# Optimization experiments

Measured on AMD Instinct MI355X. Metric: run time of the kernel, lower is better.

The kernel has to match this reference:

```python
import jax, jax.numpy as jnp
import numpy as np

N = 100000
E = 640000
D_IN = 128
D_OUT = 128
EPS = 0.0


def setup_inputs() -> dict:
    key = jax.random.key(0)
    k1, k2, k3, k4, k5, k6 = jax.random.split(key, 6)
    x = jax.random.normal(k1, (N, D_IN), dtype=jnp.float32)
    edge_index = jax.random.randint(k2, (2, E), 0, N, dtype=jnp.int64)
    # MLP params (Linear(in,out) -> ReLU -> Linear(out,out)), PyTorch-style init scale
    s1 = 1.0 / np.sqrt(D_IN)
    s2 = 1.0 / np.sqrt(D_OUT)
    W1 = jax.random.uniform(k3, (D_IN, D_OUT), minval=-s1, maxval=s1, dtype=jnp.float32)
    b1 = jax.random.uniform(k4, (D_OUT,), minval=-s1, maxval=s1, dtype=jnp.float32)
    W2 = jax.random.uniform(k5, (D_OUT, D_OUT), minval=-s2, maxval=s2, dtype=jnp.float32)
    b2 = jax.random.uniform(k6, (D_OUT,), minval=-s2, maxval=s2, dtype=jnp.float32)
    return {"x": x, "edge_index": edge_index, "W1": W1, "b1": b1, "W2": W2, "b2": b2}


def reference(x, edge_index, W1, b1, W2, b2):
    row, col = edge_index[0], edge_index[1]
    # gather source features, scatter-add into destination nodes
    aggregated = jax.ops.segment_sum(x[row], col, num_segments=N)  # [N, D_IN]
    h = (1.0 + EPS) * x + aggregated
    h = jnp.maximum(h @ W1 + b1, 0.0)
    return h @ W2 + b2
```

## Files before the change

### kernel.cpp

```cpp
#include <hip/hip_runtime.h>

#define NN 100000
#define EE 640000
#define DD 128
#define NB 391

typedef short bf16x8 __attribute__((ext_vector_type(8)));
typedef float f32x4 __attribute__((ext_vector_type(4)));

__device__ __forceinline__ unsigned short f2bf(float f) {
    union { float f; unsigned int u; } a; a.f = f;
    unsigned int u = a.u + 0x7fffu + ((a.u >> 16) & 1u);
    return (unsigned short)(u >> 16);
}

__device__ __forceinline__ int wave_incl_scan(int v, int lane) {
#pragma unroll
    for (int d = 1; d < 64; d <<= 1) {
        int u = __shfl_up(v, d, 64);
        if (lane >= d) v += u;
    }
    return v;
}

__global__ __launch_bounds__(256) void k_hist(const int* __restrict__ ei,
                                              int* __restrict__ deg) {
    int e = blockIdx.x * 256 + threadIdx.x;
    if (e >= EE) return;
    atomicAdd(&deg[ei[EE + e]], 1);
}

__global__ __launch_bounds__(256) void k_scan1(const int* __restrict__ deg,
                                               int* __restrict__ bsum) {
    int i = blockIdx.x * 256 + threadIdx.x;
    int v = (i < NN) ? deg[i] : 0;
#pragma unroll
    for (int d = 32; d; d >>= 1) v += __shfl_down(v, d, 64);
    __shared__ int wsum[4];
    if ((threadIdx.x & 63) == 0) wsum[threadIdx.x >> 6] = v;
    __syncthreads();
    if (threadIdx.x == 0) bsum[blockIdx.x] = wsum[0] + wsum[1] + wsum[2] + wsum[3];
}

__global__ __launch_bounds__(512) void k_scan2(int* __restrict__ bsum,
                                               int* __restrict__ offs) {
    int t = threadIdx.x, lane = t & 63, w = t >> 6;
    int v = (t < NB) ? bsum[t] : 0;
    int s = wave_incl_scan(v, lane);
    __shared__ int wsum[8];
    if (lane == 63) wsum[w] = s;
    __syncthreads();
    int off = 0;
    for (int k = 0; k < w; ++k) off += wsum[k];
    if (t < NB) bsum[t] = off + s - v;
    if (t == 0) offs[NN] = EE;
}

__global__ __launch_bounds__(256) void k_scan3(const int* __restrict__ deg,
                                               const int* __restrict__ bsum,
                                               int* __restrict__ offs) {
    int t = threadIdx.x, lane = t & 63, w = t >> 6;
    int i = blockIdx.x * 256 + t;
    int v = (i < NN) ? deg[i] : 0;
    int s = wave_incl_scan(v, lane);
    __shared__ int wsum[4];
    if (lane == 63) wsum[w] = s;
    __syncthreads();
    int off = bsum[blockIdx.x];
    for (int k = 0; k < w; ++k) off += wsum[k];
    if (i < NN) offs[i] = off + s - v;
}

__global__ __launch_bounds__(256) void k_fill(const int* __restrict__ ei,
                                              int* __restrict__ deg,
                                              const int* __restrict__ offs,
                                              int* __restrict__ bucket) {
    int e = blockIdx.x * 256 + threadIdx.x;
    if (e >= EE) return;
    int r = ei[e];
    int c = ei[EE + e];
    int p = atomicSub(&deg[c], 1) - 1;
    bucket[offs[c] + p] = r;
}

__global__ __launch_bounds__(256) void k_gather(const float* __restrict__ x,
                                                const int* __restrict__ offs,
                                                const int* __restrict__ bucket,
                                                float* __restrict__ h0) {
    int gid = blockIdx.x * 256 + threadIdx.x;
    int n = gid >> 6;
    if (n >= NN) return;
    int lane = gid & 63;
    const float2* xr = reinterpret_cast<const float2*>(x);
    float2 acc = xr[(size_t)n * 64 + lane];
    int j = offs[n], jend = offs[n + 1];
    for (; j + 1 < jend; j += 2) {
        int a = bucket[j], b = bucket[j + 1];
        float2 va = xr[(size_t)a * 64 + lane];
        float2 vb = xr[(size_t)b * 64 + lane];
        acc.x += va.x + vb.x;
        acc.y += va.y + vb.y;
    }
    if (j < jend) {
        int a = bucket[j];
        float2 va = xr[(size_t)a * 64 + lane];
        acc.x += va.x;
        acc.y += va.y;
    }
    reinterpret_cast<float2*>(h0)[(size_t)n * 64 + lane] = acc;
}

__global__ __launch_bounds__(256) void k_prep(const float* __restrict__ W1,
                                              const float* __restrict__ W2,
                                              unsigned short* __restrict__ w1t,
                                              unsigned short* __restrict__ w2t) {
    int idx = blockIdx.x * 256 + threadIdx.x;
    if (idx >= 2 * DD * DD) return;
    const float* W = (idx < DD * DD) ? W1 : W2;
    unsigned short* O = (idx < DD * DD) ? w1t : w2t;
    int i = idx & (DD * DD - 1);
    int n = i >> 7, k = i & (DD - 1);
    O[i] = f2bf(W[k * DD + n]);
}

__global__ __launch_bounds__(256, 2) void k_mlp(const float* __restrict__ h0,
                                                const unsigned short* __restrict__ w1t,
                                                const unsigned short* __restrict__ w2t,
                                                const float* __restrict__ b1,
                                                const float* __restrict__ b2,
                                                float* __restrict__ out) {
    __shared__ unsigned short lds[DD * DD];
    const int t  = threadIdx.x;
    const int w  = t >> 6, l = t & 63;
    const int wr = w >> 1, wc = w & 1;
    const int hi = l >> 4, lo = l & 15;
    const long base_row = (long)blockIdx.x * 128;

    bf16x8 bw1[4][4];
#pragma unroll
    for (int n = 0; n < 4; ++n)
#pragma unroll
        for (int k = 0; k < 4; ++k)
            bw1[n][k] = *reinterpret_cast<const bf16x8*>(
                w1t + (wc * 64 + n * 16 + lo) * DD + k * 32 + hi * 8);

#pragma unroll
    for (int it = 0; it < 16; ++it) {
        int idx = it * 1024 + t * 4;
        int row = idx >> 7, col = idx & (DD - 1);
        long g = base_row + row;
        float4 v = make_float4(0.f, 0.f, 0.f, 0.f);
        if (g < NN) v = *reinterpret_cast<const float4*>(h0 + g * DD + col);
        unsigned int u0 = (unsigned)f2bf(v.x) | ((unsigned)f2bf(v.y) << 16);
        unsigned int u1 = (unsigned)f2bf(v.z) | ((unsigned)f2bf(v.w) << 16);
        int byte = (row * 256 + col * 2) ^ ((row & 7) << 4);
        *reinterpret_cast<uint2*>(reinterpret_cast<char*>(lds) + byte) = make_uint2(u0, u1);
    }
    __syncthreads();

    const f32x4 zero = {0.f, 0.f, 0.f, 0.f};

    f32x4 acc[4][4];
#pragma unroll
    for (int m = 0; m < 4; ++m)
#pragma unroll
        for (int n = 0; n < 4; ++n) acc[m][n] = zero;
#pragma unroll
    for (int m = 0; m < 4; ++m) {
        bf16x8 a[4];
        int r = wr * 64 + m * 16 + lo;
#pragma unroll
        for (int k = 0; k < 4; ++k) {
            int byte = (r * 256 + k * 64 + hi * 16) ^ ((r & 7) << 4);
            a[k] = *reinterpret_cast<const bf16x8*>(reinterpret_cast<const char*>(lds) + byte);
        }
#pragma unroll
        for (int n = 0; n < 4; ++n)
#pragma unroll
            for (int k = 0; k < 4; ++k)
                acc[m][n] = __builtin_amdgcn_mfma_f32_16x16x32_bf16(a[k], bw1[n][k], acc[m][n], 0, 0, 0);
    }
    __syncthreads();

    float bias1[4];
#pragma unroll
    for (int n = 0; n < 4; ++n) bias1[n] = b1[wc * 64 + n * 16 + lo];
#pragma unroll
    for (int m = 0; m < 4; ++m)
#pragma unroll
        for (int n = 0; n < 4; ++n)
#pragma unroll
            for (int g = 0; g < 4; ++g) {
                int row = wr * 64 + m * 16 + hi * 4 + g;
                int col = wc * 64 + n * 16 + lo;
                float v = fmaxf(acc[m][n][g] + bias1[n], 0.f);
                int byte = (row * 256 + col * 2) ^ ((row & 7) << 4);
                *reinterpret_cast<unsigned short*>(reinterpret_cast<char*>(lds) + byte) = f2bf(v);
            }
    __syncthreads();

    bf16x8 bw2[4][4];
#pragma unroll
    for (int n = 0; n < 4; ++n)
#pragma unroll
        for (int k = 0; k < 4; ++k)
            bw2[n][k] = *reinterpret_cast<const bf16x8*>(
                w2t + (wc * 64 + n * 16 + lo) * DD + k * 32 + hi * 8);

    f32x4 acc2[4][4];
#pragma unroll
    for (int m = 0; m < 4; ++m)
#pragma unroll
        for (int n = 0; n < 4; ++n) acc2[m][n] = zero;
#pragma unroll
    for (int m = 0; m < 4; ++m) {
        bf16x8 a[4];
        int r = wr * 64 + m * 16 + lo;
#pragma unroll
        for (int k = 0; k < 4; ++k) {
            int byte = (r * 256 + k * 64 + hi * 16) ^ ((r & 7) << 4);
            a[k] = *reinterpret_cast<const bf16x8*>(reinterpret_cast<const char*>(lds) + byte);
        }
#pragma unroll
        for (int n = 0; n < 4; ++n)
#pragma unroll
            for (int k = 0; k < 4; ++k)
                acc2[m][n] = __builtin_amdgcn_mfma_f32_16x16x32_bf16(a[k], bw2[n][k], acc2[m][n], 0, 0, 0);
    }

    float bias2[4];
#pragma unroll
    for (int n = 0; n < 4; ++n) bias2[n] = b2[wc * 64 + n * 16 + lo];
#pragma unroll
    for (int m = 0; m < 4; ++m)
#pragma unroll
        for (int n = 0; n < 4; ++n)
#pragma unroll
            for (int g = 0; g < 4; ++g) {
                long row = base_row + wr * 64 + m * 16 + hi * 4 + g;
                if (row < NN)
                    out[row * DD + wc * 64 + n * 16 + lo] = acc2[m][n][g] + bias2[n];
            }
}

extern "C" void kernel_launch(void* const* d_in, const int* in_sizes, int n_in,
                              void* d_out, int out_size, void* d_ws, size_t ws_size,
                              hipStream_t stream) {
    const float* x  = (const float*)d_in[0];
    const int*   ei = (const int*)d_in[1];
    const float* W1 = (const float*)d_in[2];
    const float* b1 = (const float*)d_in[3];
    const float* W2 = (const float*)d_in[4];
    const float* b2 = (const float*)d_in[5];
    float* out = (float*)d_out;

    char* ws = (char*)d_ws;
    float* h0 = (float*)ws;
    unsigned short* w1t = (unsigned short*)(ws + 51200000);
    unsigned short* w2t = w1t + DD * DD;
    int* deg    = (int*)(ws + 51200000 + 65536);
    int* offs   = deg + NN;
    int* bsum   = offs + NN + 1;
    int* bucket = bsum + 512;

    hipMemsetAsync(deg, 0, NN * sizeof(int), stream);
    k_prep<<<(2 * DD * DD + 255) / 256, 256, 0, stream>>>(W1, W2, w1t, w2t);
    k_hist<<<(EE + 255) / 256, 256, 0, stream>>>(ei, deg);
    k_scan1<<<NB, 256, 0, stream>>>(deg, bsum);
    k_scan2<<<1, 512, 0, stream>>>(bsum, offs);
    k_scan3<<<NB, 256, 0, stream>>>(deg, bsum, offs);
    k_fill<<<(EE + 255) / 256, 256, 0, stream>>>(ei, deg, offs, bucket);
    k_gather<<<(NN * 64 + 255) / 256, 256, 0, stream>>>(x, offs, bucket, h0);
    k_mlp<<<(NN + 127) / 128, 256, 0, stream>>>(h0, w1t, w2t, b1, b2, out);
}
```

Measured before the change: 268.8 us.

## Fuse neighbor gather into MLP kernel and gather from bf16 copy of x

Converts x to bf16 once in a combined setup kernel, which also transposes the weights and zeroes the degree array, replacing the memset and the prep kernel. The gather-sum is moved into the MLP kernel, so each block aggregates its 128 rows straight into LDS and the fp32 h0 intermediate is never written to or read back from global memory. Reading bf16 neighbor rows halves the gather traffic. The cost is reduced precision: x is rounded to bf16 before the sum rather than after, and the gather now runs at the MLP kernel's lower occupancy (launch bounds 256,2 with a 32 KB LDS tile).

```diff
diff --git a/kernel.cpp b/kernel.cpp
--- a/kernel.cpp
+++ b/kernel.cpp
@@ -5,6 +5,10 @@
 #define DD 128
 #define NB 391
 
+#define CVT_BLKS  12500
+#define PREP_BLKS 128
+#define ZERO_BLKS 98
+
 typedef short bf16x8 __attribute__((ext_vector_type(8)));
 typedef float f32x4 __attribute__((ext_vector_type(4)));
 
@@ -21,6 +25,34 @@
         if (lane >= d) v += u;
     }
     return v;
+}
+
+__global__ __launch_bounds__(256) void k_setup(const float* __restrict__ x,
+                                               const float* __restrict__ W1,
+                                               const float* __restrict__ W2,
+                                               unsigned short* __restrict__ xb,
+                                               unsigned short* __restrict__ w1t,
+                                               unsigned short* __restrict__ w2t,
+                                               int* __restrict__ deg) {
+    int b = blockIdx.x, t = threadIdx.x;
+    if (b < CVT_BLKS) {
+        int i = (b * 256 + t) * 4;
+        float4 v = *reinterpret_cast<const float4*>(x + i);
+        unsigned int u0 = (unsigned)f2bf(v.x) | ((unsigned)f2bf(v.y) << 16);
+        unsigned int u1 = (unsigned)f2bf(v.z) | ((unsigned)f2bf(v.w) << 16);
+        *reinterpret_cast<uint2*>(xb + i) = make_uint2(u0, u1);
+    } else if (b < CVT_BLKS + PREP_BLKS) {
+        int idx = (b - CVT_BLKS) * 256 + t;
+        const float* W = (idx < DD * DD) ? W1 : W2;
+        unsigned short* O = (idx < DD * DD) ? w1t : w2t;
+        int i = idx & (DD * DD - 1);
+        int n = i >> 7, k = i & (DD - 1);
+        O[i] = f2bf(W[k * DD + n]);
+    } else {
+        int idx = (b - CVT_BLKS - PREP_BLKS) * 256 + t;
+        if (idx < 25000)
+            reinterpret_cast<int4*>(deg)[idx] = make_int4(0, 0, 0, 0);
+    }
 }
 
 __global__ __launch_bounds__(256) void k_hist(const int* __restrict__ ei,
@@ -83,58 +115,55 @@
     bucket[offs[c] + p] = r;
 }
 
-__global__ __launch_bounds__(256) void k_gather(const float* __restrict__ x,
-                                                const int* __restrict__ offs,
-                                                const int* __restrict__ bucket,
-                                                float* __restrict__ h0) {
-    int gid = blockIdx.x * 256 + threadIdx.x;
-    int n = gid >> 6;
-    if (n >= NN) return;
-    int lane = gid & 63;
-    const float2* xr = reinterpret_cast<const float2*>(x);
-    float2 acc = xr[(size_t)n * 64 + lane];
-    int j = offs[n], jend = offs[n + 1];
-    for (; j + 1 < jend; j += 2) {
-        int a = bucket[j], b = bucket[j + 1];
-        float2 va = xr[(size_t)a * 64 + lane];
-        float2 vb = xr[(size_t)b * 64 + lane];
-        acc.x += va.x + vb.x;
-        acc.y += va.y + vb.y;
-    }
-    if (j < jend) {
-        int a = bucket[j];
-        float2 va = xr[(size_t)a * 64 + lane];
-        acc.x += va.x;
-        acc.y += va.y;
-    }
-    reinterpret_cast<float2*>(h0)[(size_t)n * 64 + lane] = acc;
-}
-
-__global__ __launch_bounds__(256) void k_prep(const float* __restrict__ W1,
-                                              const float* __restrict__ W2,
-                                              unsigned short* __restrict__ w1t,
-                                              unsigned short* __restrict__ w2t) {
-    int idx = blockIdx.x * 256 + threadIdx.x;
-    if (idx >= 2 * DD * DD) return;
-    const float* W = (idx < DD * DD) ? W1 : W2;
-    unsigned short* O = (idx < DD * DD) ? w1t : w2t;
-    int i = idx & (DD * DD - 1);
-    int n = i >> 7, k = i & (DD - 1);
-    O[i] = f2bf(W[k * DD + n]);
-}
-
-__global__ __launch_bounds__(256, 2) void k_mlp(const float* __restrict__ h0,
-                                                const unsigned short* __restrict__ w1t,
-                                                const unsigned short* __restrict__ w2t,
-                                                const float* __restrict__ b1,
-                                                const float* __restrict__ b2,
-                                                float* __restrict__ out) {
+__global__ __launch_bounds__(256, 2) void k_fused(const unsigned short* __restrict__ xb,
+                                                  const int* __restrict__ offs,
+                                                  const int* __restrict__ bucket,
+                                                  const unsigned short* __restrict__ w1t,
+                                                  const unsigned short* __restrict__ w2t,
+                                                  const float* __restrict__ b1,
+                                                  const float* __restrict__ b2,
+                                                  float* __restrict__ out) {
     __shared__ unsigned short lds[DD * DD];
     const int t  = threadIdx.x;
     const int w  = t >> 6, l = t & 63;
     const int wr = w >> 1, wc = w & 1;
     const int hi = l >> 4, lo = l & 15;
     const long base_row = (long)blockIdx.x * 128;
+    const unsigned int* xr = reinterpret_cast<const unsigned int*>(xb);
+
+    for (int i = 0; i < 32; ++i) {
+        int r = w * 32 + i;
+        long n = base_row + r;
+        float ax = 0.f, ay = 0.f;
+        if (n < NN) {
+            unsigned int u = xr[(size_t)n * 64 + l];
+            ax = __uint_as_float(u << 16);
+            ay = __uint_as_float(u & 0xffff0000u);
+            int j = offs[n], je = offs[n + 1];
+            for (; j + 3 < je; j += 4) {
+                int a0 = bucket[j], a1 = bucket[j + 1], a2 = bucket[j + 2], a3 = bucket[j + 3];
+                unsigned int u0 = xr[(size_t)a0 * 64 + l];
+                unsigned int u1 = xr[(size_t)a1 * 64 + l];
+                unsigned int u2 = xr[(size_t)a2 * 64 + l];
+                unsigned int u3 = xr[(size_t)a3 * 64 + l];
+                ax += __uint_as_float(u0 << 16) + __uint_as_float(u1 << 16)
+                    + __uint_as_float(u2 << 16) + __uint_as_float(u3 << 16);
+                ay += __uint_as_float(u0 & 0xffff0000u) + __uint_as_float(u1 & 0xffff0000u)
+                    + __uint_as_float(u2 & 0xffff0000u) + __uint_as_float(u3 & 0xffff0000u);
+            }
+            for (; j < je; ++j) {
+                unsigned int u = xr[(size_t)bucket[j] * 64 + l];
+                ax += __uint_as_float(u << 16);
+                ay += __uint_as_float(u & 0xffff0000u);
+            }
+        }
+        unsigned int p = (unsigned)f2bf(ax) | ((unsigned)f2bf(ay) << 16);
+        int byte = (r * 256 + l * 4) ^ ((r & 7) << 4);
+        *reinterpret_cast<unsigned int*>(reinterpret_cast<char*>(lds) + byte) = p;
+    }
+    __syncthreads();
+
+    const f32x4 zero = {0.f, 0.f, 0.f, 0.f};
 
     bf16x8 bw1[4][4];
 #pragma unroll
@@ -143,22 +172,6 @@
         for (int k = 0; k < 4; ++k)
             bw1[n][k] = *reinterpret_cast<const bf16x8*>(
                 w1t + (wc * 64 + n * 16 + lo) * DD + k * 32 + hi * 8);
-
-#pragma unroll
-    for (int it = 0; it < 16; ++it) {
-        int idx = it * 1024 + t * 4;
-        int row = idx >> 7, col = idx & (DD - 1);
-        long g = base_row + row;
-        float4 v = make_float4(0.f, 0.f, 0.f, 0.f);
-        if (g < NN) v = *reinterpret_cast<const float4*>(h0 + g * DD + col);
-        unsigned int u0 = (unsigned)f2bf(v.x) | ((unsigned)f2bf(v.y) << 16);
-        unsigned int u1 = (unsigned)f2bf(v.z) | ((unsigned)f2bf(v.w) << 16);
-        int byte = (row * 256 + col * 2) ^ ((row & 7) << 4);
-        *reinterpret_cast<uint2*>(reinterpret_cast<char*>(lds) + byte) = make_uint2(u0, u1);
-    }
-    __syncthreads();
-
-    const f32x4 zero = {0.f, 0.f, 0.f, 0.f};
 
     f32x4 acc[4][4];
 #pragma unroll
@@ -255,21 +268,19 @@
     float* out = (float*)d_out;
 
     char* ws = (char*)d_ws;
-    float* h0 = (float*)ws;
-    unsigned short* w1t = (unsigned short*)(ws + 51200000);
+    unsigned short* xb  = (unsigned short*)ws;
+    unsigned short* w1t = (unsigned short*)(ws + 25600000);
     unsigned short* w2t = w1t + DD * DD;
-    int* deg    = (int*)(ws + 51200000 + 65536);
+    int* deg    = (int*)(ws + 25600000 + 65536);
     int* offs   = deg + NN;
     int* bsum   = offs + NN + 1;
     int* bucket = bsum + 512;
 
-    hipMemsetAsync(deg, 0, NN * sizeof(int), stream);
-    k_prep<<<(2 * DD * DD + 255) / 256, 256, 0, stream>>>(W1, W2, w1t, w2t);
+    k_setup<<<CVT_BLKS + PREP_BLKS + ZERO_BLKS, 256, 0, stream>>>(x, W1, W2, xb, w1t, w2t, deg);
     k_hist<<<(EE + 255) / 256, 256, 0, stream>>>(ei, deg);
     k_scan1<<<NB, 256, 0, stream>>>(deg, bsum);
     k_scan2<<<1, 512, 0, stream>>>(bsum, offs);
     k_scan3<<<NB, 256, 0, stream>>>(deg, bsum, offs);
     k_fill<<<(EE + 255) / 256, 256, 0, stream>>>(ei, deg, offs, bucket);
-    k_gather<<<(NN * 64 + 255) / 256, 256, 0, stream>>>(x, offs, bucket, h0);
-    k_mlp<<<(NN + 127) / 128, 256, 0, stream>>>(h0, w1t, w2t, b1, b2, out);
-}
+    k_fused<<<(NN + 127) / 128, 256, 0, stream>>>(xb, offs, bucket, w1t, w2t, b1, b2, out);
+}
```

After: 323.4 us. 20.3% more time.
